# Kernel tuning notes

Measured on AMD Instinct MI355X. Metric: run time of the kernel, lower is better.

The kernel has to match this reference:

```python
import jax, jax.numpy as jnp
import numpy as np

D_MODEL = 1024
NUM_HEADS = 16
DEPTH = D_MODEL // NUM_HEADS


def setup_inputs() -> dict:
    key = jax.random.key(0)
    ks = jax.random.split(key, 11)
    B, S = 4, 2048
    scale = 1.0 / np.sqrt(D_MODEL)
    inp = {
        "query": jax.random.normal(ks[0], (B, S, D_MODEL), jnp.float32),
        "key": jax.random.normal(ks[1], (B, S, D_MODEL), jnp.float32),
        "value": jax.random.normal(ks[2], (B, S, D_MODEL), jnp.float32),
        # Linear params (torch nn.Linear: y = x @ W.T + b); store W as [out, in]
        "wq_w": jax.random.normal(ks[3], (D_MODEL, D_MODEL), jnp.float32) * scale,
        "wq_b": jnp.zeros((D_MODEL,), jnp.float32),
        "wk_w": jax.random.normal(ks[4], (D_MODEL, D_MODEL), jnp.float32) * scale,
        "wk_b": jnp.zeros((D_MODEL,), jnp.float32),
        "wv_w": jax.random.normal(ks[5], (D_MODEL, D_MODEL), jnp.float32) * scale,
        "wv_b": jnp.zeros((D_MODEL,), jnp.float32),
        "dense_w": jax.random.normal(ks[6], (D_MODEL, D_MODEL), jnp.float32) * scale,
        "dense_b": jnp.zeros((D_MODEL,), jnp.float32),
    }
    return inp


def _split_heads(x, B):
    # [B, S, D] -> [B, H, S, depth]
    return x.reshape(B, -1, NUM_HEADS, DEPTH).transpose(0, 2, 1, 3)


def reference(query, key, value, wq_w, wq_b, wk_w, wk_b, wv_w, wv_b, dense_w, dense_b):
    B = query.shape[0]
    q = _split_heads(query @ wq_w.T + wq_b, B)   # [B,H,Sq,depth]
    k = _split_heads(key @ wk_w.T + wk_b, B)     # [B,H,Sk,depth]
    v = _split_heads(value @ wv_w.T + wv_b, B)   # [B,H,Sk,depth]
    scores = jnp.einsum("bhqd,bhkd->bhqk", q, k) / jnp.sqrt(jnp.float32(DEPTH)).astype(q.dtype)
    attn = jax.nn.softmax(scores, axis=-1)
    out = jnp.einsum("bhqk,bhkd->bhqd", attn, v)  # [B,H,Sq,depth]
    out = out.transpose(0, 2, 1, 3).reshape(B, -1, D_MODEL)
    return out @ dense_w.T + dense_b
```

## Files before the change

### kernel.cpp

```cpp
#include <hip/hip_runtime.h>
#include <hip/hip_bf16.h>
#include <stdint.h>


#define SEQ    2048
#define DEPTH  64
#define HEADS  16
#define NMODEL 1024
#define MROWS  8192

typedef __bf16 bf16x8 __attribute__((ext_vector_type(8)));
typedef float  f32x4  __attribute__((ext_vector_type(4)));

__device__ __forceinline__ unsigned short f32_bf16(float f) {
    union { float f; unsigned int u; } c; c.f = f;
    unsigned int u = c.u + 0x7FFFu + ((c.u >> 16) & 1u);
    return (unsigned short)(u >> 16);
}

__device__ __forceinline__ void gload16(const unsigned short* g, unsigned short* l) {
    __builtin_amdgcn_global_load_lds(
        (const __attribute__((address_space(1))) unsigned int*)g,
        (__attribute__((address_space(3))) unsigned int*)l, 16, 0, 0);
}

__global__ __launch_bounds__(256) void cvt3_kernel(
    const float* __restrict__ a, const float* __restrict__ b, const float* __restrict__ c,
    unsigned short* __restrict__ oa, unsigned short* __restrict__ ob,
    unsigned short* __restrict__ oc, int n4)
{
    const float* in; unsigned short* out;
    if (blockIdx.y == 0) { in = a; out = oa; }
    else if (blockIdx.y == 1) { in = b; out = ob; }
    else { in = c; out = oc; }
    int i = blockIdx.x * 256 + threadIdx.x;
    if (i < n4) {
        float4 f = ((const float4*)in)[i];
        ushort4 o;
        o.x = f32_bf16(f.x); o.y = f32_bf16(f.y);
        o.z = f32_bf16(f.z); o.w = f32_bf16(f.w);
        ((ushort4*)out)[i] = o;
    }
}

__global__ __launch_bounds__(256) void cvt4_kernel(
    const float* __restrict__ a, const float* __restrict__ b,
    const float* __restrict__ c, const float* __restrict__ d,
    unsigned short* __restrict__ oa, unsigned short* __restrict__ ob,
    unsigned short* __restrict__ oc, unsigned short* __restrict__ od, int n4)
{
    const float* in; unsigned short* out;
    if (blockIdx.y == 0) { in = a; out = oa; }
    else if (blockIdx.y == 1) { in = b; out = ob; }
    else if (blockIdx.y == 2) { in = c; out = oc; }
    else { in = d; out = od; }
    int i = blockIdx.x * 256 + threadIdx.x;
    if (i < n4) {
        float4 f = ((const float4*)in)[i];
        ushort4 o;
        o.x = f32_bf16(f.x); o.y = f32_bf16(f.y);
        o.z = f32_bf16(f.z); o.w = f32_bf16(f.w);
        ((ushort4*)out)[i] = o;
    }
}

__device__ __forceinline__ void gemm256_core(
    const unsigned short* __restrict__ A, const unsigned short* __restrict__ W,
    const float* __restrict__ bias, void* __restrict__ outp,
    int mode, float scale, int m0, int n0,
    unsigned short* __restrict__ Alds, unsigned short* __restrict__ Blds)
{
    const int tid  = threadIdx.x;
    const int wave = tid >> 6, lane = tid & 63;
    const int l15  = lane & 15, quad = lane >> 4;
    const int wr   = wave >> 1, wc = wave & 1;
    const int swz  = l15 & 7;
    const int K    = 1024;

    f32x4 acc[4][4] = {};

    const int trow = tid >> 3;
    const int tg   = ((tid & 7) ^ (trow & 7)) << 3;
    const unsigned short* Asrc[2][2];
    const unsigned short* Bsrc[2];
    #pragma unroll
    for (int u = 0; u < 2; ++u) {
        #pragma unroll
        for (int s = 0; s < 2; ++s)
            Asrc[u][s] = A + (size_t)(m0 + u * 128 + s * 64 + trow) * K + tg;
        Bsrc[u] = W + (size_t)(n0 + u * 64 + trow) * K + tg;
    }

    auto STAGE = [&](int buf, int kt2, int u) {
        gload16(Asrc[u][0] + kt2 * 64, Alds + buf * 16384 + (u * 128 + wave * 8) * 64);
        gload16(Asrc[u][1] + kt2 * 64, Alds + buf * 16384 + (u * 128 + 64 + wave * 8) * 64);
        gload16(Bsrc[u]    + kt2 * 64, Blds + buf * 8192  + (u * 64 + wave * 8) * 64);
    };

    STAGE(0, 0, 0);
    STAGE(0, 0, 1);
    asm volatile("s_waitcnt vmcnt(0)" ::: "memory");
    __builtin_amdgcn_s_barrier();

    for (int kt = 0; kt < 16; ++kt) {
        const int cur = kt & 1;
        const unsigned short* Ab = Alds + cur * 16384;
        const unsigned short* Bb = Blds + cur * 8192;
        const int arow = wr * 64 + l15;
        const int brow = wc * 64 + l15;
        const bool pre = (kt + 1 < 16);
        bf16x8 bfr[4], af0, af1;

        {
            const int pg = ((quad ^ swz) << 3);
            bfr[0] = *(const bf16x8*)&Bb[(brow)      * 64 + pg];
            bfr[1] = *(const bf16x8*)&Bb[(brow + 16) * 64 + pg];
            bfr[2] = *(const bf16x8*)&Bb[(brow + 32) * 64 + pg];
            bfr[3] = *(const bf16x8*)&Bb[(brow + 48) * 64 + pg];
            af0    = *(const bf16x8*)&Ab[(arow)      * 64 + pg];
            af1    = *(const bf16x8*)&Ab[(arow + 16) * 64 + pg];
            if (pre) STAGE(cur ^ 1, kt + 1, 0);
            __builtin_amdgcn_s_barrier();
            __builtin_amdgcn_s_setprio(1);
            #pragma unroll
            for (int j = 0; j < 4; ++j)
                acc[0][j] = __builtin_amdgcn_mfma_f32_16x16x32_bf16(af0, bfr[j], acc[0][j], 0, 0, 0);
            #pragma unroll
            for (int j = 0; j < 4; ++j)
                acc[1][j] = __builtin_amdgcn_mfma_f32_16x16x32_bf16(af1, bfr[j], acc[1][j], 0, 0, 0);
            __builtin_amdgcn_s_setprio(0);
            __builtin_amdgcn_s_barrier();
        }
        {
            const int pg = ((quad ^ swz) << 3);
            af0 = *(const bf16x8*)&Ab[(arow + 32) * 64 + pg];
            af1 = *(const bf16x8*)&Ab[(arow + 48) * 64 + pg];
            if (pre) STAGE(cur ^ 1, kt + 1, 1);
            __builtin_amdgcn_s_barrier();
            __builtin_amdgcn_s_setprio(1);
            #pragma unroll
            for (int j = 0; j < 4; ++j)
                acc[2][j] = __builtin_amdgcn_mfma_f32_16x16x32_bf16(af0, bfr[j], acc[2][j], 0, 0, 0);
            #pragma unroll
            for (int j = 0; j < 4; ++j)
                acc[3][j] = __builtin_amdgcn_mfma_f32_16x16x32_bf16(af1, bfr[j], acc[3][j], 0, 0, 0);
            __builtin_amdgcn_s_setprio(0);
            __builtin_amdgcn_s_barrier();
        }
        {
            const int pg = (((4 + quad) ^ swz) << 3);
            bfr[0] = *(const bf16x8*)&Bb[(brow)      * 64 + pg];
            bfr[1] = *(const bf16x8*)&Bb[(brow + 16) * 64 + pg];
            bfr[2] = *(const bf16x8*)&Bb[(brow + 32) * 64 + pg];
            bfr[3] = *(const bf16x8*)&Bb[(brow + 48) * 64 + pg];
            af0    = *(const bf16x8*)&Ab[(arow)      * 64 + pg];
            af1    = *(const bf16x8*)&Ab[(arow + 16) * 64 + pg];
            __builtin_amdgcn_s_barrier();
            __builtin_amdgcn_s_setprio(1);
            #pragma unroll
            for (int j = 0; j < 4; ++j)
                acc[0][j] = __builtin_amdgcn_mfma_f32_16x16x32_bf16(af0, bfr[j], acc[0][j], 0, 0, 0);
            #pragma unroll
            for (int j = 0; j < 4; ++j)
                acc[1][j] = __builtin_amdgcn_mfma_f32_16x16x32_bf16(af1, bfr[j], acc[1][j], 0, 0, 0);
            __builtin_amdgcn_s_setprio(0);
            __builtin_amdgcn_s_barrier();
        }
        {
            const int pg = (((4 + quad) ^ swz) << 3);
            af0 = *(const bf16x8*)&Ab[(arow + 32) * 64 + pg];
            af1 = *(const bf16x8*)&Ab[(arow + 48) * 64 + pg];
            __builtin_amdgcn_s_barrier();
            __builtin_amdgcn_s_setprio(1);
            #pragma unroll
            for (int j = 0; j < 4; ++j)
                acc[2][j] = __builtin_amdgcn_mfma_f32_16x16x32_bf16(af0, bfr[j], acc[2][j], 0, 0, 0);
            #pragma unroll
            for (int j = 0; j < 4; ++j)
                acc[3][j] = __builtin_amdgcn_mfma_f32_16x16x32_bf16(af1, bfr[j], acc[3][j], 0, 0, 0);
            __builtin_amdgcn_s_setprio(0);
            asm volatile("s_waitcnt vmcnt(0)" ::: "memory");
            __builtin_amdgcn_s_barrier();
        }
    }

    #pragma unroll
    for (int i = 0; i < 4; ++i) {
        #pragma unroll
        for (int j = 0; j < 4; ++j) {
            const int col = n0 + wc * 64 + j * 16 + l15;
            const int row_b = m0 + wr * 64 + i * 16 + quad * 4;
            if (mode == 2) {
                const int colp = (col & ~31)
                               | (col & 3)
                               | (((col >> 4) & 1) << 2)
                               | (((col >> 2) & 3) << 3);
                #pragma unroll
                for (int r = 0; r < 4; ++r) {
                    const int row = row_b + r;
                    ((unsigned short*)outp)[(size_t)row * MROWS + colp] =
                        f32_bf16(acc[i][j][r] + bias[row]);
                }
            } else if (mode == 0) {
                const float bv = bias[col];
                #pragma unroll
                for (int r = 0; r < 4; ++r)
                    ((float*)outp)[(size_t)(row_b + r) * NMODEL + col] = acc[i][j][r] + bv;
            } else {
                const float bv = bias[col];
                const int h_ = col >> 6, d_ = col & 63;
                #pragma unroll
                for (int r = 0; r < 4; ++r) {
                    const int row = row_b + r;
                    const int b_ = row >> 11, s_ = row & 2047;
                    ((unsigned short*)outp)[(((size_t)(b_ * HEADS + h_) * SEQ + s_) << 6) + d_] =
                        f32_bf16((acc[i][j][r] + bv) * scale);
                }
            }
        }
    }
}

__global__ __launch_bounds__(512, 2) void gemm_qkv(
    const unsigned short* __restrict__ qb,  const unsigned short* __restrict__ wqb,
    const float* __restrict__ bq, unsigned short* __restrict__ Qp,
    const unsigned short* __restrict__ kb,  const unsigned short* __restrict__ wkb,
    const float* __restrict__ bk, unsigned short* __restrict__ Kpj,
    const unsigned short* __restrict__ wvb, const unsigned short* __restrict__ vb,
    const float* __restrict__ bv, unsigned short* __restrict__ Vtg,
    float qscale)
{
    __shared__ unsigned short Alds[2 * 256 * 64];
    __shared__ unsigned short Blds[2 * 128 * 64];
    const int o = blockIdx.x, z = blockIdx.y;
    const int sid = (o & 7) * 32 + (o >> 3);
    if (z == 0) {
        gemm256_core(qb, wqb, bq, Qp, 1, qscale, (sid >> 3) * 256, (sid & 7) * 128, Alds, Blds);
    } else if (z == 1) {
        gemm256_core(kb, wkb, bk, Kpj, 1, 1.0f, (sid >> 3) * 256, (sid & 7) * 128, Alds, Blds);
    } else {
        gemm256_core(wvb, vb, bv, Vtg, 2, 1.0f, (sid & 3) * 256, (sid >> 2) * 128, Alds, Blds);
    }
}

__global__ __launch_bounds__(512, 2) void gemm_dense(
    const unsigned short* __restrict__ A, const unsigned short* __restrict__ W,
    const float* __restrict__ bias, float* __restrict__ out)
{
    __shared__ unsigned short Alds[2 * 256 * 64];
    __shared__ unsigned short Blds[2 * 128 * 64];
    const int o = blockIdx.x;
    const int sid = (o & 7) * 32 + (o >> 3);
    gemm256_core(A, W, bias, out, 0, 1.0f, (sid >> 3) * 256, (sid & 7) * 128, Alds, Blds);
}

__global__ __launch_bounds__(256, 2) void attn_fwd(
    const unsigned short* __restrict__ Qp,
    const unsigned short* __restrict__ Kp,
    const unsigned short* __restrict__ Vtg,
    unsigned short* __restrict__ Op)
{
    __shared__ unsigned short Klds[2 * 64 * 64];
    __shared__ unsigned short Vlds[2 * 64 * 64];
    const int tid  = threadIdx.x;
    const int wave = tid >> 6, lane = tid & 63;
    const int l15  = lane & 15, quad = lane >> 4;
    const int swz  = l15 & 7;
    const int bh   = blockIdx.y;
    const int b_   = bh >> 4, h_ = bh & 15;
    const int q0   = blockIdx.x * 256;

    const unsigned short* Qb = Qp + (size_t)bh * SEQ * DEPTH;
    const unsigned short* Kb = Kp + (size_t)bh * SEQ * DEPTH;
    const unsigned short* Vb = Vtg + (size_t)h_ * DEPTH * MROWS + (size_t)b_ * SEQ;

    const int srow = (wave << 3) + (lane >> 3);
    const int scg  = (lane & 7) ^ ((lane >> 3) & 7);

    const unsigned short* Kg0 = Kb + (size_t)srow * DEPTH + scg * 8;
    const unsigned short* Kg1 = Kb + (size_t)(srow + 32) * DEPTH + scg * 8;
    const unsigned short* Vg0 = Vb + (size_t)srow * MROWS + scg * 8;
    const unsigned short* Vg1 = Vb + (size_t)(srow + 32) * MROWS + scg * 8;

    bf16x8 qf[4][2];
    #pragma unroll
    for (int i = 0; i < 4; ++i)
        #pragma unroll
        for (int kc = 0; kc < 2; ++kc)
            qf[i][kc] = *(const bf16x8*)(Qb + (size_t)(q0 + wave * 64 + i * 16 + l15) * DEPTH
                                         + kc * 32 + quad * 8);

    union { bf16x8 v; unsigned short s[8]; } uo;
    #pragma unroll
    for (int j = 0; j < 8; ++j) uo.s[j] = 0x3F80;
    const bf16x8 ones = uo.v;

    f32x4 Ot[4][4] = {};
    f32x4 lacc[4]  = {};

    auto STAGE = [&](int buf, int kt) {
        unsigned short* KW = &Klds[buf * 4096 + wave * 512];
        unsigned short* VW = &Vlds[buf * 4096 + wave * 512];
        gload16(Kg0 + (size_t)kt * 4096, KW);
        gload16(Kg1 + (size_t)kt * 4096, KW + 2048);
        gload16(Vg0 + kt * 64, VW);
        gload16(Vg1 + kt * 64, VW + 2048);
    };

    STAGE(0, 0);
    asm volatile("s_waitcnt vmcnt(0)" ::: "memory");
    __builtin_amdgcn_s_barrier();

    for (int kt = 0; kt < SEQ / 64; ++kt) {
        const int cur = kt & 1;
        if (kt + 1 < SEQ / 64) STAGE(cur ^ 1, kt + 1);

        const unsigned short* Kc = &Klds[cur * 4096];

        #pragma unroll
        for (int half = 0; half < 2; ++half) {
            __builtin_amdgcn_s_setprio(1);
            const int r0 = (2 * half) * 16 + l15;
            const int r1 = (2 * half + 1) * 16 + l15;
            bf16x8 ka0 = *(const bf16x8*)&Kc[r0 * 64 + ((quad ^ swz) << 3)];
            bf16x8 ka1 = *(const bf16x8*)&Kc[r0 * 64 + (((4 + quad) ^ swz) << 3)];
            bf16x8 kb0 = *(const bf16x8*)&Kc[r1 * 64 + ((quad ^ swz) << 3)];
            bf16x8 kb1 = *(const bf16x8*)&Kc[r1 * 64 + (((4 + quad) ^ swz) << 3)];
            f32x4 S0[4], S1[4];
            #pragma unroll
            for (int i = 0; i < 4; ++i) {
                S0[i] = f32x4{};
                S0[i] = __builtin_amdgcn_mfma_f32_16x16x32_bf16(ka0, qf[i][0], S0[i], 0, 0, 0);
                S0[i] = __builtin_amdgcn_mfma_f32_16x16x32_bf16(ka1, qf[i][1], S0[i], 0, 0, 0);
                S1[i] = f32x4{};
                S1[i] = __builtin_amdgcn_mfma_f32_16x16x32_bf16(kb0, qf[i][0], S1[i], 0, 0, 0);
                S1[i] = __builtin_amdgcn_mfma_f32_16x16x32_bf16(kb1, qf[i][1], S1[i], 0, 0, 0);
            }
            __builtin_amdgcn_s_setprio(0);

            bf16x8 pfh[4];
            #pragma unroll
            for (int i = 0; i < 4; ++i) {
                float e0 = __builtin_amdgcn_exp2f(S0[i][0]);
                float e1 = __builtin_amdgcn_exp2f(S0[i][1]);
                float e2 = __builtin_amdgcn_exp2f(S0[i][2]);
                float e3 = __builtin_amdgcn_exp2f(S0[i][3]);
                float e4 = __builtin_amdgcn_exp2f(S1[i][0]);
                float e5 = __builtin_amdgcn_exp2f(S1[i][1]);
                float e6 = __builtin_amdgcn_exp2f(S1[i][2]);
                float e7 = __builtin_amdgcn_exp2f(S1[i][3]);
                union { bf16x8 v; __hip_bfloat162 h[4]; } up;
                up.h[0] = __float22bfloat162_rn(make_float2(e0, e1));
                up.h[1] = __float22bfloat162_rn(make_float2(e2, e3));
                up.h[2] = __float22bfloat162_rn(make_float2(e4, e5));
                up.h[3] = __float22bfloat162_rn(make_float2(e6, e7));
                pfh[i] = up.v;
            }

            __builtin_amdgcn_s_setprio(1);
            lacc[0] = __builtin_amdgcn_mfma_f32_16x16x32_bf16(ones, pfh[0], lacc[0], 0, 0, 0);
            lacc[1] = __builtin_amdgcn_mfma_f32_16x16x32_bf16(ones, pfh[1], lacc[1], 0, 0, 0);
            lacc[2] = __builtin_amdgcn_mfma_f32_16x16x32_bf16(ones, pfh[2], lacc[2], 0, 0, 0);
            lacc[3] = __builtin_amdgcn_mfma_f32_16x16x32_bf16(ones, pfh[3], lacc[3], 0, 0, 0);
            #pragma unroll
            for (int dd = 0; dd < 4; ++dd) {
                bf16x8 vf = *(const bf16x8*)&Vlds[cur * 4096 +
                            (dd * 16 + l15) * 64 + (((half * 4 + quad) ^ swz) << 3)];
                #pragma unroll
                for (int i = 0; i < 4; ++i)
                    Ot[i][dd] = __builtin_amdgcn_mfma_f32_16x16x32_bf16(vf, pfh[i], Ot[i][dd], 0, 0, 0);
            }
            __builtin_amdgcn_s_setprio(0);
        }

        asm volatile("s_waitcnt vmcnt(0)" ::: "memory");
        __builtin_amdgcn_s_barrier();
    }

    #pragma unroll
    for (int i = 0; i < 4; ++i) {
        const float inv = 1.0f / lacc[i][0];
        const int row = b_ * SEQ + q0 + wave * 64 + i * 16 + l15;
        #pragma unroll
        for (int dd = 0; dd < 4; ++dd) {
            ushort4 ov;
            ov.x = f32_bf16(Ot[i][dd][0] * inv);
            ov.y = f32_bf16(Ot[i][dd][1] * inv);
            ov.z = f32_bf16(Ot[i][dd][2] * inv);
            ov.w = f32_bf16(Ot[i][dd][3] * inv);
            const int col = h_ * 64 + dd * 16 + quad * 4;
            *(ushort4*)&Op[(size_t)row * NMODEL + col] = ov;
        }
    }
}

extern "C" void kernel_launch(void* const* d_in, const int* in_sizes, int n_in,
                              void* d_out, int out_size, void* d_ws, size_t ws_size,
                              hipStream_t stream) {
    const float* q  = (const float*)d_in[0];
    const float* k  = (const float*)d_in[1];
    const float* v  = (const float*)d_in[2];
    const float* wq = (const float*)d_in[3];
    const float* bq = (const float*)d_in[4];
    const float* wk = (const float*)d_in[5];
    const float* bk = (const float*)d_in[6];
    const float* wv = (const float*)d_in[7];
    const float* bv = (const float*)d_in[8];
    const float* wd = (const float*)d_in[9];
    const float* bd = (const float*)d_in[10];

    char* ws = (char*)d_ws;
    size_t off = 0;
    auto alloc = [&](size_t bytes) { char* p = ws + off; off += bytes; return p; };
    const size_t ACT = (size_t)MROWS * NMODEL * 2;
    const size_t WGT = (size_t)NMODEL * NMODEL * 2;

    unsigned short* qb   = (unsigned short*)alloc(ACT);
    unsigned short* kb   = (unsigned short*)alloc(ACT);
    unsigned short* vb   = (unsigned short*)alloc(ACT);
    unsigned short* wqb  = (unsigned short*)alloc(WGT);
    unsigned short* wkb  = (unsigned short*)alloc(WGT);
    unsigned short* wvb  = (unsigned short*)alloc(WGT);
    unsigned short* wdb  = (unsigned short*)alloc(WGT);
    unsigned short* Qp   = (unsigned short*)alloc(ACT);
    unsigned short* Kpj  = (unsigned short*)alloc(ACT);
    unsigned short* Vtg  = (unsigned short*)alloc(ACT);
    unsigned short* attn = (unsigned short*)alloc(ACT);

    const int nAct4 = MROWS * NMODEL / 4;
    const int nWgt4 = NMODEL * NMODEL / 4;
    cvt3_kernel<<<dim3(nAct4 / 256, 3), 256, 0, stream>>>(q, k, v, qb, kb, vb, nAct4);
    cvt4_kernel<<<dim3(nWgt4 / 256, 4), 256, 0, stream>>>(wq, wk, wv, wd,
                                                          wqb, wkb, wvb, wdb, nWgt4);

    const float SC = 0.18033688011112042f;
    gemm_qkv<<<dim3(256, 3), 512, 0, stream>>>(qb, wqb, bq, Qp,
                                               kb, wkb, bk, Kpj,
                                               wvb, vb, bv, Vtg, SC);

    attn_fwd<<<dim3(SEQ / 256, 64), 256, 0, stream>>>(Qp, Kpj, Vtg, attn);

    gemm_dense<<<256, 512, 0, stream>>>(attn, wdb, bd, (float*)d_out);
}
```

Before: 330.6 us.

## Triple-buffer GEMM k-loop with one barrier per tile and merge conversion kernels

The shared GEMM core moves from double buffering with four barriers per k-tile to a three-stage LDS ring. It prefetches two tiles ahead and waits with vmcnt(6), so only one barrier per k-tile remains, and all A/B fragments for each half-k step are loaded before a 4x4 MFMA burst. This targets barrier stalls and exposed global-load latency in the projection and output GEMMs. In exchange, LDS per block grows to 144KB, which limits residency to one block per CU, and fragment register pressure rises. The two fp32-to-bf16 conversion launches are also merged into one 7-slice launch, where the weight slices over-launch blocks that simply exit.

```diff
diff --git a/kernel.cpp b/kernel.cpp
--- a/kernel.cpp
+++ b/kernel.cpp
@@ -24,36 +24,26 @@
         (__attribute__((address_space(3))) unsigned int*)l, 16, 0, 0);
 }
 
-__global__ __launch_bounds__(256) void cvt3_kernel(
-    const float* __restrict__ a, const float* __restrict__ b, const float* __restrict__ c,
-    unsigned short* __restrict__ oa, unsigned short* __restrict__ ob,
-    unsigned short* __restrict__ oc, int n4)
+__global__ __launch_bounds__(256) void cvt7_kernel(
+    const float* __restrict__ a0, const float* __restrict__ a1, const float* __restrict__ a2,
+    const float* __restrict__ w0, const float* __restrict__ w1,
+    const float* __restrict__ w2, const float* __restrict__ w3,
+    unsigned short* __restrict__ oa0, unsigned short* __restrict__ oa1,
+    unsigned short* __restrict__ oa2,
+    unsigned short* __restrict__ ow0, unsigned short* __restrict__ ow1,
+    unsigned short* __restrict__ ow2, unsigned short* __restrict__ ow3,
+    int n4a, int n4w)
 {
-    const float* in; unsigned short* out;
-    if (blockIdx.y == 0) { in = a; out = oa; }
-    else if (blockIdx.y == 1) { in = b; out = ob; }
-    else { in = c; out = oc; }
-    int i = blockIdx.x * 256 + threadIdx.x;
-    if (i < n4) {
-        float4 f = ((const float4*)in)[i];
-        ushort4 o;
-        o.x = f32_bf16(f.x); o.y = f32_bf16(f.y);
-        o.z = f32_bf16(f.z); o.w = f32_bf16(f.w);
-        ((ushort4*)out)[i] = o;
-    }
-}
-
-__global__ __launch_bounds__(256) void cvt4_kernel(
-    const float* __restrict__ a, const float* __restrict__ b,
-    const float* __restrict__ c, const float* __restrict__ d,
-    unsigned short* __restrict__ oa, unsigned short* __restrict__ ob,
-    unsigned short* __restrict__ oc, unsigned short* __restrict__ od, int n4)
-{
-    const float* in; unsigned short* out;
-    if (blockIdx.y == 0) { in = a; out = oa; }
-    else if (blockIdx.y == 1) { in = b; out = ob; }
-    else if (blockIdx.y == 2) { in = c; out = oc; }
-    else { in = d; out = od; }
+    const float* in; unsigned short* out; int n4;
+    switch (blockIdx.y) {
+        case 0: in = a0; out = oa0; n4 = n4a; break;
+        case 1: in = a1; out = oa1; n4 = n4a; break;
+        case 2: in = a2; out = oa2; n4 = n4a; break;
+        case 3: in = w0; out = ow0; n4 = n4w; break;
+        case 4: in = w1; out = ow1; n4 = n4w; break;
+        case 5: in = w2; out = ow2; n4 = n4w; break;
+        default: in = w3; out = ow3; n4 = n4w; break;
+    }
     int i = blockIdx.x * 256 + threadIdx.x;
     if (i < n4) {
         float4 f = ((const float4*)in)[i];
@@ -91,97 +81,72 @@
         Bsrc[u] = W + (size_t)(n0 + u * 64 + trow) * K + tg;
     }
 
-    auto STAGE = [&](int buf, int kt2, int u) {
-        gload16(Asrc[u][0] + kt2 * 64, Alds + buf * 16384 + (u * 128 + wave * 8) * 64);
-        gload16(Asrc[u][1] + kt2 * 64, Alds + buf * 16384 + (u * 128 + 64 + wave * 8) * 64);
-        gload16(Bsrc[u]    + kt2 * 64, Blds + buf * 8192  + (u * 64 + wave * 8) * 64);
+    auto STAGE = [&](int buf, int kt2) {
+        unsigned short* Ad = Alds + buf * 16384;
+        unsigned short* Bd = Blds + buf * 8192;
+        gload16(Asrc[0][0] + kt2 * 64, Ad + (      wave * 8) * 64);
+        gload16(Asrc[0][1] + kt2 * 64, Ad + ( 64 + wave * 8) * 64);
+        gload16(Asrc[1][0] + kt2 * 64, Ad + (128 + wave * 8) * 64);
+        gload16(Asrc[1][1] + kt2 * 64, Ad + (192 + wave * 8) * 64);
+        gload16(Bsrc[0]    + kt2 * 64, Bd + (      wave * 8) * 64);
+        gload16(Bsrc[1]    + kt2 * 64, Bd + ( 64 + wave * 8) * 64);
     };
 
-    STAGE(0, 0, 0);
-    STAGE(0, 0, 1);
-    asm volatile("s_waitcnt vmcnt(0)" ::: "memory");
+    STAGE(0, 0);
+    STAGE(1, 1);
+    asm volatile("s_waitcnt vmcnt(6)" ::: "memory");
     __builtin_amdgcn_s_barrier();
 
+    const int arow = wr * 64 + l15;
+    const int brow = wc * 64 + l15;
+
     for (int kt = 0; kt < 16; ++kt) {
-        const int cur = kt & 1;
-        const unsigned short* Ab = Alds + cur * 16384;
-        const unsigned short* Bb = Blds + cur * 8192;
-        const int arow = wr * 64 + l15;
-        const int brow = wc * 64 + l15;
-        const bool pre = (kt + 1 < 16);
-        bf16x8 bfr[4], af0, af1;
-
+        const unsigned short* Ab = Alds + (kt % 3) * 16384;
+        const unsigned short* Bb = Blds + (kt % 3) * 8192;
+
+        bf16x8 a0[4], b0[4];
         {
             const int pg = ((quad ^ swz) << 3);
-            bfr[0] = *(const bf16x8*)&Bb[(brow)      * 64 + pg];
-            bfr[1] = *(const bf16x8*)&Bb[(brow + 16) * 64 + pg];
-            bfr[2] = *(const bf16x8*)&Bb[(brow + 32) * 64 + pg];
-            bfr[3] = *(const bf16x8*)&Bb[(brow + 48) * 64 + pg];
-            af0    = *(const bf16x8*)&Ab[(arow)      * 64 + pg];
-            af1    = *(const bf16x8*)&Ab[(arow + 16) * 64 + pg];
-            if (pre) STAGE(cur ^ 1, kt + 1, 0);
-            __builtin_amdgcn_s_barrier();
-            __builtin_amdgcn_s_setprio(1);
             #pragma unroll
             for (int j = 0; j < 4; ++j)
-                acc[0][j] = __builtin_amdgcn_mfma_f32_16x16x32_bf16(af0, bfr[j], acc[0][j], 0, 0, 0);
+                b0[j] = *(const bf16x8*)&Bb[(brow + j * 16) * 64 + pg];
+            #pragma unroll
+            for (int i = 0; i < 4; ++i)
+                a0[i] = *(const bf16x8*)&Ab[(arow + i * 16) * 64 + pg];
+        }
+        if (kt + 2 < 16) STAGE((kt + 2) % 3, kt + 2);
+
+        __builtin_amdgcn_s_setprio(1);
+        #pragma unroll
+        for (int i = 0; i < 4; ++i)
             #pragma unroll
             for (int j = 0; j < 4; ++j)
-                acc[1][j] = __builtin_amdgcn_mfma_f32_16x16x32_bf16(af1, bfr[j], acc[1][j], 0, 0, 0);
-            __builtin_amdgcn_s_setprio(0);
-            __builtin_amdgcn_s_barrier();
-        }
-        {
-            const int pg = ((quad ^ swz) << 3);
-            af0 = *(const bf16x8*)&Ab[(arow + 32) * 64 + pg];
-            af1 = *(const bf16x8*)&Ab[(arow + 48) * 64 + pg];
-            if (pre) STAGE(cur ^ 1, kt + 1, 1);
-            __builtin_amdgcn_s_barrier();
-            __builtin_amdgcn_s_setprio(1);
-            #pragma unroll
-            for (int j = 0; j < 4; ++j)
-                acc[2][j] = __builtin_amdgcn_mfma_f32_16x16x32_bf16(af0, bfr[j], acc[2][j], 0, 0, 0);
-            #pragma unroll
-            for (int j = 0; j < 4; ++j)
-                acc[3][j] = __builtin_amdgcn_mfma_f32_16x16x32_bf16(af1, bfr[j], acc[3][j], 0, 0, 0);
-            __builtin_amdgcn_s_setprio(0);
-            __builtin_amdgcn_s_barrier();
-        }
+                acc[i][j] = __builtin_amdgcn_mfma_f32_16x16x32_bf16(a0[i], b0[j], acc[i][j], 0, 0, 0);
+        __builtin_amdgcn_s_setprio(0);
+
+        bf16x8 a1[4], b1[4];
         {
             const int pg = (((4 + quad) ^ swz) << 3);
-            bfr[0] = *(const bf16x8*)&Bb[(brow)      * 64 + pg];
-            bfr[1] = *(const bf16x8*)&Bb[(brow + 16) * 64 + pg];
-            bfr[2] = *(const bf16x8*)&Bb[(brow + 32) * 64 + pg];
-            bfr[3] = *(const bf16x8*)&Bb[(brow + 48) * 64 + pg];
-            af0    = *(const bf16x8*)&Ab[(arow)      * 64 + pg];
-            af1    = *(const bf16x8*)&Ab[(arow + 16) * 64 + pg];
-            __builtin_amdgcn_s_barrier();
-            __builtin_amdgcn_s_setprio(1);
             #pragma unroll
             for (int j = 0; j < 4; ++j)
-                acc[0][j] = __builtin_amdgcn_mfma_f32_16x16x32_bf16(af0, bfr[j], acc[0][j], 0, 0, 0);
+                b1[j] = *(const bf16x8*)&Bb[(brow + j * 16) * 64 + pg];
+            #pragma unroll
+            for (int i = 0; i < 4; ++i)
+                a1[i] = *(const bf16x8*)&Ab[(arow + i * 16) * 64 + pg];
+        }
+        __builtin_amdgcn_s_setprio(1);
+        #pragma unroll
+        for (int i = 0; i < 4; ++i)
             #pragma unroll
             for (int j = 0; j < 4; ++j)
-                acc[1][j] = __builtin_amdgcn_mfma_f32_16x16x32_bf16(af1, bfr[j], acc[1][j], 0, 0, 0);
-            __builtin_amdgcn_s_setprio(0);
-            __builtin_amdgcn_s_barrier();
-        }
-        {
-            const int pg = (((4 + quad) ^ swz) << 3);
-            af0 = *(const bf16x8*)&Ab[(arow + 32) * 64 + pg];
-            af1 = *(const bf16x8*)&Ab[(arow + 48) * 64 + pg];
-            __builtin_amdgcn_s_barrier();
-            __builtin_amdgcn_s_setprio(1);
-            #pragma unroll
-            for (int j = 0; j < 4; ++j)
-                acc[2][j] = __builtin_amdgcn_mfma_f32_16x16x32_bf16(af0, bfr[j], acc[2][j], 0, 0, 0);
-            #pragma unroll
-            for (int j = 0; j < 4; ++j)
-                acc[3][j] = __builtin_amdgcn_mfma_f32_16x16x32_bf16(af1, bfr[j], acc[3][j], 0, 0, 0);
-            __builtin_amdgcn_s_setprio(0);
+                acc[i][j] = __builtin_amdgcn_mfma_f32_16x16x32_bf16(a1[i], b1[j], acc[i][j], 0, 0, 0);
+        __builtin_amdgcn_s_setprio(0);
+
+        if (kt + 2 < 16)
+            asm volatile("s_waitcnt vmcnt(6)" ::: "memory");
+        else
             asm volatile("s_waitcnt vmcnt(0)" ::: "memory");
-            __builtin_amdgcn_s_barrier();
-        }
+        __builtin_amdgcn_s_barrier();
     }
 
     #pragma unroll
@@ -230,8 +195,8 @@
     const float* __restrict__ bv, unsigned short* __restrict__ Vtg,
     float qscale)
 {
-    __shared__ unsigned short Alds[2 * 256 * 64];
-    __shared__ unsigned short Blds[2 * 128 * 64];
+    __shared__ unsigned short Alds[3 * 256 * 64];
+    __shared__ unsigned short Blds[3 * 128 * 64];
     const int o = blockIdx.x, z = blockIdx.y;
     const int sid = (o & 7) * 32 + (o >> 3);
     if (z == 0) {
@@ -247,8 +212,8 @@
     const unsigned short* __restrict__ A, const unsigned short* __restrict__ W,
     const float* __restrict__ bias, float* __restrict__ out)
 {
-    __shared__ unsigned short Alds[2 * 256 * 64];
-    __shared__ unsigned short Blds[2 * 128 * 64];
+    __shared__ unsigned short Alds[3 * 256 * 64];
+    __shared__ unsigned short Blds[3 * 128 * 64];
     const int o = blockIdx.x;
     const int sid = (o & 7) * 32 + (o >> 3);
     gemm256_core(A, W, bias, out, 0, 1.0f, (sid >> 3) * 256, (sid & 7) * 128, Alds, Blds);
@@ -429,9 +394,8 @@
 
     const int nAct4 = MROWS * NMODEL / 4;
     const int nWgt4 = NMODEL * NMODEL / 4;
-    cvt3_kernel<<<dim3(nAct4 / 256, 3), 256, 0, stream>>>(q, k, v, qb, kb, vb, nAct4);
-    cvt4_kernel<<<dim3(nWgt4 / 256, 4), 256, 0, stream>>>(wq, wk, wv, wd,
-                                                          wqb, wkb, wvb, wdb, nWgt4);
+    cvt7_kernel<<<dim3(nAct4 / 256, 7), 256, 0, stream>>>(
+        q, k, v, wq, wk, wv, wd, qb, kb, vb, wqb, wkb, wvb, wdb, nAct4, nWgt4);
 
     const float SC = 0.18033688011112042f;
     gemm_qkv<<<dim3(256, 3), 512, 0, stream>>>(qb, wqb, bq, Qp,
```

Result: faster. 315.0 us (-4.7%).
